# Kernel tuning notes

Measured on AMD Instinct MI355X. Metric: run time of the kernel, lower is better.

## Reference

```python
import jax, jax.numpy as jnp
import numpy as np

B, N, C = 4, 2048, 768
H = 12
D = C // H  # head_dim = 64
SCALE = D ** -0.5


def setup_inputs() -> dict:
    key = jax.random.key(0)
    ks = jax.random.split(key, 9)
    x_q = jax.random.normal(ks[0], (B, N, C), dtype=jnp.float32)
    x_k = jax.random.normal(ks[1], (B, N, C), dtype=jnp.float32)
    x_v = jax.random.normal(ks[2], (B, N, C), dtype=jnp.float32)
    x_u = jax.random.uniform(ks[3], (B, N, C), dtype=jnp.float32)
    s = C ** -0.5
    Wq = jax.random.normal(ks[4], (C, C), dtype=jnp.float32) * s
    Wk = jax.random.normal(ks[5], (C, C), dtype=jnp.float32) * s
    Wv = jax.random.normal(ks[6], (C, C), dtype=jnp.float32) * s
    Wp = jax.random.normal(ks[7], (C, C), dtype=jnp.float32) * s
    bp = jax.random.normal(ks[8], (C,), dtype=jnp.float32) * 0.01
    return {"x_q": x_q, "x_k": x_k, "x_v": x_v, "x_u": x_u,
            "Wq": Wq, "Wk": Wk, "Wv": Wv, "Wp": Wp, "bp": bp}


def reference(x_q, x_k, x_v, x_u, Wq, Wk, Wv, Wp, bp):
    # Linear projections (torch Linear: y = x @ W.T), split into heads [B,H,N,D]
    def to_heads(x, W):
        y = jnp.einsum('bnc,oc->bno', x, W)
        return y.reshape(B, N, H, D).transpose(0, 2, 1, 3)
    q = to_heads(x_q, Wq) * SCALE
    k = to_heads(x_k, Wk)
    v = to_heads(x_v, Wv)
    # Scores [B,H,N,N]
    attn = jnp.einsum('bhqd,bhkd->bhqk', q, k)
    # Uncertainty map: per-query scalar (mean over channels), broadcast over keys & heads
    uc = jnp.mean(x_u, axis=-1)  # [B,N]
    attn = attn * uc[:, None, :, None]
    attn = jax.nn.softmax(attn, axis=-1)
    out = jnp.einsum('bhqk,bhkd->bhqd', attn, v)
    out = out.transpose(0, 2, 1, 3).reshape(B, N, C)
    return jnp.einsum('bnc,oc->bno', out, Wp) + bp
```

## Files before the change

kernel.cpp:

```cpp
#include <hip/hip_runtime.h>
#include <hip/hip_bf16.h>
#include <cstdint>

#define B_ 4
#define N_ 2048
#define C_ 768
#define H_ 12
#define D_ 64

typedef __bf16 bf16x8 __attribute__((ext_vector_type(8)));
typedef float f32x4 __attribute__((ext_vector_type(4)));

__device__ __forceinline__ unsigned f2bs(float x) {
  unsigned u = __builtin_bit_cast(unsigned, x);
  unsigned r = (u + 0x7fffu + ((u >> 16) & 1u)) >> 16;
  return r;
}

__device__ __forceinline__ bf16x8 ldb8(const unsigned short* p) {
  return __builtin_bit_cast(bf16x8, *(const uint4*)p);
}

__device__ __forceinline__ f32x4 mfma16(bf16x8 a, bf16x8 b, f32x4 c) {
  return __builtin_amdgcn_mfma_f32_16x16x32_bf16(a, b, c, 0, 0, 0);
}

__device__ __forceinline__ void async16(const unsigned short* g, unsigned short* l) {
  __builtin_amdgcn_global_load_lds(
      (const __attribute__((address_space(1))) unsigned int*)g,
      (__attribute__((address_space(3))) unsigned int*)l, 16, 0, 0);
}

__global__ void convx_kernel(const float* __restrict__ s0, const float* __restrict__ s1,
                             const float* __restrict__ s2,
                             unsigned short* __restrict__ d0, unsigned short* __restrict__ d1,
                             unsigned short* __restrict__ d2) {
  const float* s; unsigned short* d;
  switch (blockIdx.y) {
    case 0: s = s0; d = d0; break;
    case 1: s = s1; d = d1; break;
    default: s = s2; d = d2; break;
  }
  int i = (blockIdx.x * 256 + threadIdx.x) * 4;
  float4 v = *(const float4*)(s + i);
  ushort4 h;
  h.x = (unsigned short)f2bs(v.x); h.y = (unsigned short)f2bs(v.y);
  h.z = (unsigned short)f2bs(v.z); h.w = (unsigned short)f2bs(v.w);
  *(ushort4*)(d + i) = h;
}

__global__ void convw_kernel(const float* __restrict__ s0, const float* __restrict__ s1,
                             const float* __restrict__ s2, const float* __restrict__ s3,
                             unsigned short* __restrict__ d0, unsigned short* __restrict__ d1,
                             unsigned short* __restrict__ d2, unsigned short* __restrict__ d3) {
  const float* s; unsigned short* d;
  switch (blockIdx.y) {
    case 0: s = s0; d = d0; break;
    case 1: s = s1; d = d1; break;
    case 2: s = s2; d = d2; break;
    default: s = s3; d = d3; break;
  }
  int i = (blockIdx.x * 256 + threadIdx.x) * 4;
  float4 v = *(const float4*)(s + i);
  ushort4 h;
  h.x = (unsigned short)f2bs(v.x); h.y = (unsigned short)f2bs(v.y);
  h.z = (unsigned short)f2bs(v.z); h.w = (unsigned short)f2bs(v.w);
  *(ushort4*)(d + i) = h;
}

__global__ void uc_kernel(const float* __restrict__ xu, float* __restrict__ uc) {
  int w = threadIdx.x >> 6, lane = threadIdx.x & 63;
  int row = blockIdx.x * 4 + w;
  const float* p = xu + (size_t)row * C_;
  float s = 0.f;
#pragma unroll
  for (int i = 0; i < 3; ++i) {
    float4 v = *(const float4*)(p + (i * 64 + lane) * 4);
    s += v.x + v.y + v.z + v.w;
  }
#pragma unroll
  for (int off = 1; off < 64; off <<= 1) s += __shfl_xor(s, off);
  if (lane == 0) uc[row] = s * (1.f / 768.f);
}

__device__ __forceinline__ void gemm_mainloop(
    const unsigned short* __restrict__ A, const unsigned short* __restrict__ W,
    int m0, int n0, unsigned short* Al, unsigned short* Bl,
    int tid, int wm, int wn, int quad, int id15, f32x4 (*acc)[4]) {
  const int wb = tid & 192;
  const int c0 = tid;
  const int r0 = c0 >> 2, o0 = (c0 & 3) << 3;
  const int c1 = 256 + tid;
  const int r1 = c1 >> 2, o1 = (c1 & 3) << 3;
  const unsigned short* a0 = A + (size_t)(m0 + r0) * C_ + o0;
  const unsigned short* a1 = A + (size_t)(m0 + r1) * C_ + o1;
  const unsigned short* b0 = W + (size_t)(n0 + r0) * C_ + o0;
  const unsigned short* b1 = W + (size_t)(n0 + r1) * C_ + o1;

  for (int kt = 0; kt < C_; kt += 32) {
    __syncthreads();
    async16(a0 + kt, Al + (size_t)wb * 8);
    async16(a1 + kt, Al + (size_t)(256 + wb) * 8);
    async16(b0 + kt, Bl + (size_t)wb * 8);
    async16(b1 + kt, Bl + (size_t)(256 + wb) * 8);
    __syncthreads();

    bf16x8 af[4], bfr[4];
#pragma unroll
    for (int i = 0; i < 4; ++i)
      af[i]  = ldb8(&Al[(wm + i * 16 + id15) * 32 + quad * 8]);
#pragma unroll
    for (int j = 0; j < 4; ++j)
      bfr[j] = ldb8(&Bl[(wn + j * 16 + id15) * 32 + quad * 8]);
#pragma unroll
    for (int i = 0; i < 4; ++i)
#pragma unroll
      for (int j = 0; j < 4; ++j)
        acc[i][j] = mfma16(af[i], bfr[j], acc[i][j]);
  }
}

__global__ __launch_bounds__(256, 3) void gemm_qkv(
    const unsigned short* __restrict__ xq, const unsigned short* __restrict__ xk,
    const unsigned short* __restrict__ xv,
    const unsigned short* __restrict__ wq, const unsigned short* __restrict__ wk,
    const unsigned short* __restrict__ wv,
    unsigned short* __restrict__ oq, unsigned short* __restrict__ ok,
    unsigned short* __restrict__ ov, const float* __restrict__ uc) {
  __shared__ __align__(16) unsigned short Al[128 * 32];
  __shared__ __align__(16) unsigned short Bl[128 * 32];
  const int tid = threadIdx.x;
  const int w = tid >> 6, lane = tid & 63, quad = lane >> 4, id15 = lane & 15;
  const int wm = (w >> 1) << 6, wn = (w & 1) << 6;
  const int m0 = blockIdx.y << 7, n0 = blockIdx.x << 7;
  const int z = blockIdx.z;

  const unsigned short* A = (z == 0) ? xq : (z == 1) ? xk : xv;
  const unsigned short* W = (z == 0) ? wq : (z == 1) ? wk : wv;

  f32x4 acc[4][4] = {};
  gemm_mainloop(A, W, m0, n0, Al, Bl, tid, wm, wn, quad, id15, acc);

#pragma unroll
  for (int i = 0; i < 4; ++i) {
#pragma unroll
    for (int j = 0; j < 4; ++j) {
#pragma unroll
      for (int r = 0; r < 4; ++r) {
        int gm = m0 + wm + i * 16 + quad * 4 + r;
        int gn = n0 + wn + j * 16 + id15;
        float v = acc[i][j][r];
        if (z == 0) {
          v *= 0.125f * uc[gm];
          oq[(size_t)gm * C_ + gn] = (unsigned short)f2bs(v);
        } else if (z == 1) {
          ok[(size_t)gm * C_ + gn] = (unsigned short)f2bs(v);
        } else {
          int b = gm >> 11, n = gm & (N_ - 1);
          ov[(size_t)(b * C_ + gn) * N_ + n] = (unsigned short)f2bs(v);
        }
      }
    }
  }
}

__global__ __launch_bounds__(256, 3) void gemm_out(
    const unsigned short* __restrict__ ao, const unsigned short* __restrict__ wp,
    float* __restrict__ out, const float* __restrict__ bias) {
  __shared__ __align__(16) unsigned short Al[128 * 32];
  __shared__ __align__(16) unsigned short Bl[128 * 32];
  const int tid = threadIdx.x;
  const int w = tid >> 6, lane = tid & 63, quad = lane >> 4, id15 = lane & 15;
  const int wm = (w >> 1) << 6, wn = (w & 1) << 6;
  const int m0 = blockIdx.y << 7, n0 = blockIdx.x << 7;

  f32x4 acc[4][4] = {};
  gemm_mainloop(ao, wp, m0, n0, Al, Bl, tid, wm, wn, quad, id15, acc);

#pragma unroll
  for (int i = 0; i < 4; ++i) {
#pragma unroll
    for (int j = 0; j < 4; ++j) {
#pragma unroll
      for (int r = 0; r < 4; ++r) {
        int gm = m0 + wm + i * 16 + quad * 4 + r;
        int gn = n0 + wn + j * 16 + id15;
        out[(size_t)gm * C_ + gn] = acc[i][j][r] + bias[gn];
      }
    }
  }
}

#define KSTR 72
#define PSTR 72
__global__ __launch_bounds__(256, 3) void attn_kernel(
    const unsigned short* __restrict__ Q, const unsigned short* __restrict__ Kk,
    const unsigned short* __restrict__ Vt, unsigned short* __restrict__ O) {
  __shared__ __align__(16) unsigned short Kl[64 * KSTR];
  __shared__ __align__(16) unsigned short Vl[64 * KSTR];
  __shared__ __align__(16) unsigned short Pl[8][16 * PSTR];

  const int tid = threadIdx.x;
  const int w = tid >> 6, lane = tid & 63, quad = lane >> 4, id15 = lane & 15;
  const int bh = blockIdx.y;
  const int b = bh / H_, h = bh % H_;
  const int q0 = blockIdx.x * 128 + w * 32;

  bf16x8 qf[2][2];
#pragma unroll
  for (int rg = 0; rg < 2; ++rg)
#pragma unroll
    for (int kb = 0; kb < 2; ++kb)
      qf[rg][kb] = ldb8(Q + (size_t)(b * N_ + q0 + rg * 16 + id15) * C_ + h * 64 + kb * 32 + quad * 8);

  f32x4 oacc[2][4] = {};
  float lsum[2] = {0.f, 0.f};

  const size_t kbase = (size_t)(b * N_) * C_ + h * 64;
  const size_t vbase = (size_t)(b * C_ + h * 64) * N_;
  const int srow0 = tid >> 3, srow1 = (256 + tid) >> 3;
  const int sseg0 = (tid & 7) << 3;

  unsigned short* Plw0 = &Pl[w * 2 + 0][0];
  unsigned short* Plw1 = &Pl[w * 2 + 1][0];

  for (int kc = 0; kc < N_; kc += 64) {
    __syncthreads();
    *(uint4*)&Kl[srow0 * KSTR + sseg0] = *(const uint4*)(Kk + kbase + (size_t)(kc + srow0) * C_ + sseg0);
    *(uint4*)&Kl[srow1 * KSTR + sseg0] = *(const uint4*)(Kk + kbase + (size_t)(kc + srow1) * C_ + sseg0);
    *(uint4*)&Vl[srow0 * KSTR + sseg0] = *(const uint4*)(Vt + vbase + (size_t)srow0 * N_ + kc + sseg0);
    *(uint4*)&Vl[srow1 * KSTR + sseg0] = *(const uint4*)(Vt + vbase + (size_t)srow1 * N_ + kc + sseg0);
    __syncthreads();

    f32x4 sA[4], sB[4];
#pragma unroll
    for (int cb = 0; cb < 4; ++cb) {
      f32x4 a = {}, c = {};
#pragma unroll
      for (int kb = 0; kb < 2; ++kb) {
        bf16x8 kf = ldb8(&Kl[(cb * 16 + id15) * KSTR + kb * 32 + quad * 8]);
        a = mfma16(kf, qf[0][kb], a);
        c = mfma16(kf, qf[1][kb], c);
      }
      sA[cb] = a; sB[cb] = c;
    }

#pragma unroll
    for (int rg = 0; rg < 2; ++rg) {
      f32x4* s4 = (rg == 0) ? sA : sB;
      unsigned short* Plw = (rg == 0) ? Plw0 : Plw1;
      float ls = 0.f;
#pragma unroll
      for (int cb = 0; cb < 4; ++cb) {
        float p0 = __expf(s4[cb][0]);
        float p1 = __expf(s4[cb][1]);
        float p2 = __expf(s4[cb][2]);
        float p3 = __expf(s4[cb][3]);
        ls += (p0 + p1) + (p2 + p3);
        uint2 u;
        u.x = f2bs(p0) | (f2bs(p1) << 16);
        u.y = f2bs(p2) | (f2bs(p3) << 16);
        *(uint2*)&Plw[id15 * PSTR + cb * 16 + quad * 4] = u;
      }
      lsum[rg] += ls;
    }

    bf16x8 pf[2][2];
#pragma unroll
    for (int kb = 0; kb < 2; ++kb) {
      pf[0][kb] = ldb8(&Plw0[id15 * PSTR + kb * 32 + quad * 8]);
      pf[1][kb] = ldb8(&Plw1[id15 * PSTR + kb * 32 + quad * 8]);
    }

#pragma unroll
    for (int db = 0; db < 4; ++db) {
#pragma unroll
      for (int kb = 0; kb < 2; ++kb) {
        bf16x8 vf = ldb8(&Vl[(db * 16 + id15) * KSTR + kb * 32 + quad * 8]);
        oacc[0][db] = mfma16(pf[0][kb], vf, oacc[0][db]);
        oacc[1][db] = mfma16(pf[1][kb], vf, oacc[1][db]);
      }
    }
  }

#pragma unroll
  for (int rg = 0; rg < 2; ++rg) {
    float l = lsum[rg];
    l += __shfl_xor(l, 16);
    l += __shfl_xor(l, 32);
    float linv = 1.0f / l;
#pragma unroll
    for (int r = 0; r < 4; ++r) {
      float li = __shfl(linv, quad * 4 + r);
      int n = q0 + rg * 16 + quad * 4 + r;
#pragma unroll
      for (int db = 0; db < 4; ++db)
        O[(size_t)(b * N_ + n) * C_ + h * 64 + db * 16 + id15] = (unsigned short)f2bs(oacc[rg][db][r] * li);
    }
  }
}

extern "C" void kernel_launch(void* const* d_in, const int* in_sizes, int n_in,
                              void* d_out, int out_size, void* d_ws, size_t ws_size,
                              hipStream_t stream) {
  const float* x_q = (const float*)d_in[0];
  const float* x_k = (const float*)d_in[1];
  const float* x_v = (const float*)d_in[2];
  const float* x_u = (const float*)d_in[3];
  const float* Wq  = (const float*)d_in[4];
  const float* Wk  = (const float*)d_in[5];
  const float* Wv  = (const float*)d_in[6];
  const float* Wp  = (const float*)d_in[7];
  const float* bp  = (const float*)d_in[8];

  char* ws = (char*)d_ws;
  size_t off = 0;
  auto alloc = [&](size_t bytes) {
    char* p = ws + off;
    off += (bytes + 255) & ~(size_t)255;
    return p;
  };
  unsigned short* wq16 = (unsigned short*)alloc((size_t)C_ * C_ * 2);
  unsigned short* wk16 = (unsigned short*)alloc((size_t)C_ * C_ * 2);
  unsigned short* wv16 = (unsigned short*)alloc((size_t)C_ * C_ * 2);
  unsigned short* wp16 = (unsigned short*)alloc((size_t)C_ * C_ * 2);
  float*          ucp  = (float*)alloc((size_t)B_ * N_ * 4);
  unsigned short* xq16 = (unsigned short*)alloc((size_t)B_ * N_ * C_ * 2);
  unsigned short* xk16 = (unsigned short*)alloc((size_t)B_ * N_ * C_ * 2);
  unsigned short* xv16 = (unsigned short*)alloc((size_t)B_ * N_ * C_ * 2);
  unsigned short* q_s  = (unsigned short*)alloc((size_t)B_ * N_ * C_ * 2);
  unsigned short* k_s  = (unsigned short*)alloc((size_t)B_ * N_ * C_ * 2);
  unsigned short* vT   = (unsigned short*)alloc((size_t)B_ * N_ * C_ * 2);
  unsigned short* ao   = (unsigned short*)alloc((size_t)B_ * N_ * C_ * 2);

  convx_kernel<<<dim3(6144, 3), 256, 0, stream>>>(x_q, x_k, x_v, xq16, xk16, xv16);
  convw_kernel<<<dim3(576, 4), 256, 0, stream>>>(Wq, Wk, Wv, Wp, wq16, wk16, wv16, wp16);
  uc_kernel<<<dim3(2048), 256, 0, stream>>>(x_u, ucp);
  gemm_qkv<<<dim3(6, 64, 3), 256, 0, stream>>>(xq16, xk16, xv16, wq16, wk16, wv16,
                                               q_s, k_s, vT, ucp);
  attn_kernel<<<dim3(16, 48), 256, 0, stream>>>(q_s, k_s, vT, ao);
  gemm_out<<<dim3(6, 64), 256, 0, stream>>>(ao, wp16, (float*)d_out, bp);
}
```

Measured before the change: 339.5 us.

## Use exp2 with folded log2e, MFMA row sums, truncating bf16 packing, BK=64 GEMM

The Q pre-scale now folds log2(e) into the constant so the softmax uses exp2f directly, and the bf16 packing of probabilities switches from round-to-nearest to truncation via a byte permute. Row sums are computed by an MFMA against a vector of ones using the same bf16 probabilities, which drops the per-element adds and the cross-lane shuffles at the end. Separately, the GEMM main loop doubles the K tile to 64, halving the number of barrier pairs, at the cost of twice the LDS per block. The risks are truncation bias in the probabilities and possible lower occupancy from the larger shared-memory footprint.

```diff
diff --git a/kernel.cpp b/kernel.cpp
--- a/kernel.cpp
+++ b/kernel.cpp
@@ -7,6 +7,7 @@
 #define C_ 768
 #define H_ 12
 #define D_ 64
+#define QSCALE 0.18033688011112042f
 
 typedef __bf16 bf16x8 __attribute__((ext_vector_type(8)));
 typedef float f32x4 __attribute__((ext_vector_type(4)));
@@ -88,35 +89,45 @@
     int m0, int n0, unsigned short* Al, unsigned short* Bl,
     int tid, int wm, int wn, int quad, int id15, f32x4 (*acc)[4]) {
   const int wb = tid & 192;
-  const int c0 = tid;
-  const int r0 = c0 >> 2, o0 = (c0 & 3) << 3;
-  const int c1 = 256 + tid;
-  const int r1 = c1 >> 2, o1 = (c1 & 3) << 3;
-  const unsigned short* a0 = A + (size_t)(m0 + r0) * C_ + o0;
-  const unsigned short* a1 = A + (size_t)(m0 + r1) * C_ + o1;
-  const unsigned short* b0 = W + (size_t)(n0 + r0) * C_ + o0;
-  const unsigned short* b1 = W + (size_t)(n0 + r1) * C_ + o1;
-
-  for (int kt = 0; kt < C_; kt += 32) {
+  int rows[4], cols[4];
+#pragma unroll
+  for (int s = 0; s < 4; ++s) {
+    int g = s * 256 + tid;
+    rows[s] = (g >> 2) & 127;
+    cols[s] = ((g >> 9) << 5) | ((g & 3) << 3);
+  }
+  const unsigned short* ap[4];
+  const unsigned short* bp[4];
+#pragma unroll
+  for (int s = 0; s < 4; ++s) {
+    ap[s] = A + (size_t)(m0 + rows[s]) * C_ + cols[s];
+    bp[s] = W + (size_t)(n0 + rows[s]) * C_ + cols[s];
+  }
+
+  for (int kt = 0; kt < C_; kt += 64) {
     __syncthreads();
-    async16(a0 + kt, Al + (size_t)wb * 8);
-    async16(a1 + kt, Al + (size_t)(256 + wb) * 8);
-    async16(b0 + kt, Bl + (size_t)wb * 8);
-    async16(b1 + kt, Bl + (size_t)(256 + wb) * 8);
+#pragma unroll
+    for (int s = 0; s < 4; ++s) {
+      async16(ap[s] + kt, Al + (s * 256 + wb) * 8);
+      async16(bp[s] + kt, Bl + (s * 256 + wb) * 8);
+    }
     __syncthreads();
 
-    bf16x8 af[4], bfr[4];
-#pragma unroll
-    for (int i = 0; i < 4; ++i)
-      af[i]  = ldb8(&Al[(wm + i * 16 + id15) * 32 + quad * 8]);
-#pragma unroll
-    for (int j = 0; j < 4; ++j)
-      bfr[j] = ldb8(&Bl[(wn + j * 16 + id15) * 32 + quad * 8]);
-#pragma unroll
-    for (int i = 0; i < 4; ++i)
+#pragma unroll
+    for (int kk = 0; kk < 2; ++kk) {
+      bf16x8 af[4], bfr[4];
+#pragma unroll
+      for (int i = 0; i < 4; ++i)
+        af[i]  = ldb8(&Al[kk * 4096 + (wm + i * 16 + id15) * 32 + quad * 8]);
 #pragma unroll
       for (int j = 0; j < 4; ++j)
-        acc[i][j] = mfma16(af[i], bfr[j], acc[i][j]);
+        bfr[j] = ldb8(&Bl[kk * 4096 + (wn + j * 16 + id15) * 32 + quad * 8]);
+#pragma unroll
+      for (int i = 0; i < 4; ++i)
+#pragma unroll
+        for (int j = 0; j < 4; ++j)
+          acc[i][j] = mfma16(af[i], bfr[j], acc[i][j]);
+    }
   }
 }
 
@@ -127,8 +138,8 @@
     const unsigned short* __restrict__ wv,
     unsigned short* __restrict__ oq, unsigned short* __restrict__ ok,
     unsigned short* __restrict__ ov, const float* __restrict__ uc) {
-  __shared__ __align__(16) unsigned short Al[128 * 32];
-  __shared__ __align__(16) unsigned short Bl[128 * 32];
+  __shared__ __align__(16) unsigned short Al[128 * 64];
+  __shared__ __align__(16) unsigned short Bl[128 * 64];
   const int tid = threadIdx.x;
   const int w = tid >> 6, lane = tid & 63, quad = lane >> 4, id15 = lane & 15;
   const int wm = (w >> 1) << 6, wn = (w & 1) << 6;
@@ -151,7 +162,7 @@
         int gn = n0 + wn + j * 16 + id15;
         float v = acc[i][j][r];
         if (z == 0) {
-          v *= 0.125f * uc[gm];
+          v *= QSCALE * uc[gm];
           oq[(size_t)gm * C_ + gn] = (unsigned short)f2bs(v);
         } else if (z == 1) {
           ok[(size_t)gm * C_ + gn] = (unsigned short)f2bs(v);
@@ -167,8 +178,8 @@
 __global__ __launch_bounds__(256, 3) void gemm_out(
     const unsigned short* __restrict__ ao, const unsigned short* __restrict__ wp,
     float* __restrict__ out, const float* __restrict__ bias) {
-  __shared__ __align__(16) unsigned short Al[128 * 32];
-  __shared__ __align__(16) unsigned short Bl[128 * 32];
+  __shared__ __align__(16) unsigned short Al[128 * 64];
+  __shared__ __align__(16) unsigned short Bl[128 * 64];
   const int tid = threadIdx.x;
   const int w = tid >> 6, lane = tid & 63, quad = lane >> 4, id15 = lane & 15;
   const int wm = (w >> 1) << 6, wn = (w & 1) << 6;
@@ -213,8 +224,11 @@
     for (int kb = 0; kb < 2; ++kb)
       qf[rg][kb] = ldb8(Q + (size_t)(b * N_ + q0 + rg * 16 + id15) * C_ + h * 64 + kb * 32 + quad * 8);
 
+  const uint4 onesu = {0x3F803F80u, 0x3F803F80u, 0x3F803F80u, 0x3F803F80u};
+  const bf16x8 onesf = __builtin_bit_cast(bf16x8, onesu);
+
   f32x4 oacc[2][4] = {};
-  float lsum[2] = {0.f, 0.f};
+  f32x4 lacc[2] = {};
 
   const size_t kbase = (size_t)(b * N_) * C_ + h * 64;
   const size_t vbase = (size_t)(b * C_ + h * 64) * N_;
@@ -249,20 +263,17 @@
     for (int rg = 0; rg < 2; ++rg) {
       f32x4* s4 = (rg == 0) ? sA : sB;
       unsigned short* Plw = (rg == 0) ? Plw0 : Plw1;
-      float ls = 0.f;
 #pragma unroll
       for (int cb = 0; cb < 4; ++cb) {
-        float p0 = __expf(s4[cb][0]);
-        float p1 = __expf(s4[cb][1]);
-        float p2 = __expf(s4[cb][2]);
-        float p3 = __expf(s4[cb][3]);
-        ls += (p0 + p1) + (p2 + p3);
+        unsigned p0 = __builtin_bit_cast(unsigned, exp2f(s4[cb][0]));
+        unsigned p1 = __builtin_bit_cast(unsigned, exp2f(s4[cb][1]));
+        unsigned p2 = __builtin_bit_cast(unsigned, exp2f(s4[cb][2]));
+        unsigned p3 = __builtin_bit_cast(unsigned, exp2f(s4[cb][3]));
         uint2 u;
-        u.x = f2bs(p0) | (f2bs(p1) << 16);
-        u.y = f2bs(p2) | (f2bs(p3) << 16);
+        u.x = __builtin_amdgcn_perm(p1, p0, 0x07060302u);
+        u.y = __builtin_amdgcn_perm(p3, p2, 0x07060302u);
         *(uint2*)&Plw[id15 * PSTR + cb * 16 + quad * 4] = u;
       }
-      lsum[rg] += ls;
     }
 
     bf16x8 pf[2][2];
@@ -272,6 +283,11 @@
       pf[1][kb] = ldb8(&Plw1[id15 * PSTR + kb * 32 + quad * 8]);
     }
 
+#pragma unroll
+    for (int kb = 0; kb < 2; ++kb) {
+      lacc[0] = mfma16(pf[0][kb], onesf, lacc[0]);
+      lacc[1] = mfma16(pf[1][kb], onesf, lacc[1]);
+    }
 #pragma unroll
     for (int db = 0; db < 4; ++db) {
 #pragma unroll
@@ -285,17 +301,13 @@
 
 #pragma unroll
   for (int rg = 0; rg < 2; ++rg) {
-    float l = lsum[rg];
-    l += __shfl_xor(l, 16);
-    l += __shfl_xor(l, 32);
-    float linv = 1.0f / l;
 #pragma unroll
     for (int r = 0; r < 4; ++r) {
-      float li = __shfl(linv, quad * 4 + r);
+      float linv = 1.0f / lacc[rg][r];
       int n = q0 + rg * 16 + quad * 4 + r;
 #pragma unroll
       for (int db = 0; db < 4; ++db)
-        O[(size_t)(b * N_ + n) * C_ + h * 64 + db * 16 + id15] = (unsigned short)f2bs(oacc[rg][db][r] * li);
+        O[(size_t)(b * N_ + n) * C_ + h * 64 + db * 16 + id15] = (unsigned short)f2bs(oacc[rg][db][r] * linv);
     }
   }
 }
```

After: 335.8 us. About the same (-1.1%).
